# Kernel tuning notes

Hardware: AMD Instinct MI355X
Metric: run time of the kernel (lower is better)

## Reference

```python
import jax, jax.numpy as jnp
from jax import lax
import numpy as np

CHUNK = 64


def short_conv(x, w):
    # depthwise causal conv1d: x (B,L,D), w (D,K)
    L = x.shape[1]
    K = w.shape[1]
    xp = jnp.pad(x, ((0, 0), (K - 1, 0), (0, 0)))
    return sum(xp[:, j:j + L, :] * w[:, j] for j in range(K))


def o2b_weighted_delta_rule(k, q, v, b):
    # k,q,v,b: (B,L,H,D) float32, zero initial state
    B, L, H, D = k.shape
    C = CHUNK
    Nc = L // C

    def to_chunks(t):  # (B,L,H,D) -> (Nc,B,H,C,D)
        return t.transpose(0, 2, 1, 3).reshape(B, H, Nc, C, D).transpose(2, 0, 1, 3, 4)

    Kc, Qc, Vc, Bc = map(to_chunks, (k, q, v, b))
    eyeC = jnp.eye(C, dtype=jnp.float32)
    W0 = jnp.zeros((B, H, D, D), jnp.float32)
    Cf = float(C)

    def step(carry, xs):
        W_t, W_avg = carry
        i, Ki, Qi, Vi, Bi = xs
        KiT = jnp.swapaxes(Ki, -1, -2)
        T = jnp.tril(Bi @ KiT, k=-1)                      # (B,H,C,C) strictly lower
        inv = jnp.linalg.inv(eyeC + T)
        Ui = inv @ (Vi - Bi @ W_t)                        # (B,H,C,D)
        W_new = W_t + KiT @ Ui
        ts = (i * C).astype(jnp.float32)                  # init t == 0 for all batches
        idx = jnp.arange(1, C + 1, dtype=jnp.float32) + ts  # (C,)
        cs = jnp.cumsum(idx)
        weighted_idx = idx + idx.sum() - cs
        w_i = (weighted_idx / ((1 + ts + Cf) * (ts + Cf) / 2))[:, None]  # (C,1)
        coef1 = ts / (ts + Cf) * ((1 + ts) / (1 + ts + Cf))
        coef2 = Cf / (ts + Cf) * ((ts * 2 + 1 + Cf) / (1 + ts + Cf))
        W_avg_new = coef1 * W_avg + coef2 * W_t + KiT @ (Ui * w_i)
        tri0 = (1 + ts) * ts / 2
        a = (tri0 / (tri0 + cs))[:, None]                 # (C,1)
        c = 1.0 - a
        r = cs[:, None]                                   # (C,1)
        j_idx = (cs - idx)[None, :]                       # (1,C)
        T_mat = jnp.where(r >= j_idx, (r - j_idx) / (tri0 + r), 0.0)  # (C,C)
        O_i = (Qi @ W_avg) * a + (Qi @ W_t) * c + (T_mat * (Qi @ KiT)) @ Ui
        return (W_new, W_avg_new), O_i

    (_, _), O = lax.scan(step, (W0, W0), (jnp.arange(Nc), Kc, Qc, Vc, Bc))
    # O: (Nc,B,H,C,D) -> (B,L,H,D)
    return O.transpose(1, 2, 0, 3, 4).reshape(B, H, L, D).transpose(0, 2, 1, 3)


def setup_inputs() -> dict:
    key = jax.random.key(0)
    ks = jax.random.split(key, 9)
    B, L, Dm, H = 4, 2048, 1024, 16
    Dh, K = Dm // H, 4
    s = 0.02
    return {
        'x': jax.random.normal(ks[0], (B, L, Dm), jnp.float32),
        'Wk': s * jax.random.normal(ks[1], (Dm, Dm), jnp.float32),
        'bk': jnp.zeros((Dm,), jnp.float32),
        'Wq': s * jax.random.normal(ks[2], (Dm, Dm), jnp.float32),
        'bq': jnp.zeros((Dm,), jnp.float32),
        'Wv': s * jax.random.normal(ks[3], (Dm, Dm), jnp.float32),
        'bv': jnp.zeros((Dm,), jnp.float32),
        'Wbeta': s * jax.random.normal(ks[4], (H, Dm), jnp.float32),
        'bbeta': jnp.zeros((H,), jnp.float32),
        'conv_k': 0.1 * jax.random.normal(ks[5], (Dm, K), jnp.float32),
        'conv_q': 0.1 * jax.random.normal(ks[6], (Dm, K), jnp.float32),
        'conv_v': 0.1 * jax.random.normal(ks[7], (Dm, K), jnp.float32),
        'rms_w': jnp.ones((Dh,), jnp.float32),
        'Wout': s * jax.random.normal(ks[8], (Dm, Dm), jnp.float32),
        'bout': jnp.zeros((Dm,), jnp.float32),
    }


def reference(x, Wk, bk, Wq, bq, Wv, bv, Wbeta, bbeta, conv_k, conv_q, conv_v, rms_w, Wout, bout):
    B, L, Dm = x.shape
    H = Wbeta.shape[0]
    Dh = Dm // H
    k = short_conv(x @ Wk.T + bk, conv_k)
    q = short_conv(x @ Wq.T + bq, conv_q)
    v = short_conv(x @ Wv.T + bv, conv_v)
    beta = jax.nn.sigmoid(x @ Wbeta.T + bbeta)            # (B,L,H)
    k = k.reshape(B, L, H, Dh)
    q = q.reshape(B, L, H, Dh)
    v = jax.nn.silu(v.reshape(B, L, H, Dh))
    knorm = jnp.linalg.norm(k, axis=-1, keepdims=True)
    qnorm = jnp.linalg.norm(q, axis=-1, keepdims=True)
    k = k / (knorm + 1e-6)
    q = q / (qnorm + 1e-6)
    eta = beta  # eta coefficient = 1.0, ogd_mode='deltanet'
    b = eta[..., None] * k
    v = eta[..., None] * v
    o = o2b_weighted_delta_rule(k, q, v, b)               # (B,L,H,Dh)
    o = o * jax.lax.rsqrt(jnp.mean(o * o, axis=-1, keepdims=True) + 1e-6) * rms_w
    o = o.reshape(B, L, Dm)
    return o @ Wout.T + bout
```

## Files before the change

### kernel.cpp

```cpp
#include <hip/hip_runtime.h>

typedef __attribute__((ext_vector_type(8))) short bf16x8;
typedef __attribute__((ext_vector_type(4))) float f32x4;

#define MFMA(a, b, c) __builtin_amdgcn_mfma_f32_16x16x32_bf16((a), (b), (c), 0, 0, 0)

__device__ inline unsigned short f2bf_rne(float f) {
  unsigned int u = __float_as_uint(f);
  u += 0x7FFFu + ((u >> 16) & 1u);
  return (unsigned short)(u >> 16);
}

__global__ __launch_bounds__(256) void cast_bf16_kernel(const float* __restrict__ in,
                                                        unsigned short* __restrict__ out,
                                                        int n4) {
  const int i = blockIdx.x * 256 + threadIdx.x;
  if (i >= n4) return;
  const float4 v = ((const float4*)in)[i];
  ushort4 o;
  o.x = f2bf_rne(v.x); o.y = f2bf_rne(v.y); o.z = f2bf_rne(v.z); o.w = f2bf_rne(v.w);
  ((ushort4*)out)[i] = o;
}

__global__ __launch_bounds__(256) void gemm_bf16_nt(
    const unsigned short* __restrict__ A, const unsigned short* __restrict__ Bw,
    const float* __restrict__ bias, float* __restrict__ C, int M, int N, int K) {
  __shared__ unsigned short Asl[128 * 32];
  __shared__ unsigned short Bsl[128 * 32];
  const int tid = threadIdx.x;
  const int lane = tid & 63, w = tid >> 6;
  const int bm = blockIdx.x * 128, bn = blockIdx.y * 128;
  const int wr = (w >> 1) * 64, wc = (w & 1) * 64;

  const int li0 = tid, li1 = tid + 256;
  const int ar0 = li0 >> 2, ak0 = (li0 & 3) * 8;
  const int ar1 = li1 >> 2, ak1 = (li1 & 3) * 8;
  const unsigned short* gA0 = A + (size_t)(bm + ar0) * K + ak0;
  const unsigned short* gA1 = A + (size_t)(bm + ar1) * K + ak1;
  const unsigned short* gB0 = Bw + (size_t)(bn + ar0) * K + ak0;
  const unsigned short* gB1 = Bw + (size_t)(bn + ar1) * K + ak1;
  unsigned short* lA0 = &Asl[(size_t)(w * 64) * 8];
  unsigned short* lA1 = &Asl[(size_t)(w * 64 + 256) * 8];
  unsigned short* lB0 = &Bsl[(size_t)(w * 64) * 8];
  unsigned short* lB1 = &Bsl[(size_t)(w * 64 + 256) * 8];

  f32x4 acc[4][4];
#pragma unroll
  for (int i = 0; i < 4; ++i)
#pragma unroll
    for (int j = 0; j < 4; ++j) acc[i][j] = (f32x4){0.f, 0.f, 0.f, 0.f};

  const int fr = lane & 15, kg = lane >> 4;

  for (int k0 = 0; k0 < K; k0 += 32) {
    __syncthreads();
    __builtin_amdgcn_global_load_lds((const __attribute__((address_space(1))) unsigned int*)(gA0 + k0),
                                     (__attribute__((address_space(3))) unsigned int*)lA0, 16, 0, 0);
    __builtin_amdgcn_global_load_lds((const __attribute__((address_space(1))) unsigned int*)(gA1 + k0),
                                     (__attribute__((address_space(3))) unsigned int*)lA1, 16, 0, 0);
    __builtin_amdgcn_global_load_lds((const __attribute__((address_space(1))) unsigned int*)(gB0 + k0),
                                     (__attribute__((address_space(3))) unsigned int*)lB0, 16, 0, 0);
    __builtin_amdgcn_global_load_lds((const __attribute__((address_space(1))) unsigned int*)(gB1 + k0),
                                     (__attribute__((address_space(3))) unsigned int*)lB1, 16, 0, 0);
    __syncthreads();

    bf16x8 af[4], bfr[4];
#pragma unroll
    for (int i = 0; i < 4; ++i) {
      af[i] = *(const bf16x8*)&Asl[(size_t)(wr + i * 16 + fr) * 32 + kg * 8];
      bfr[i] = *(const bf16x8*)&Bsl[(size_t)(wc + i * 16 + fr) * 32 + kg * 8];
    }
#pragma unroll
    for (int i = 0; i < 4; ++i)
#pragma unroll
      for (int j = 0; j < 4; ++j)
        acc[i][j] = MFMA(af[i], bfr[j], acc[i][j]);
  }

  const int og = lane >> 4;
#pragma unroll
  for (int j = 0; j < 4; ++j) {
    const int col = bn + wc + j * 16 + fr;
    const float bs = bias[col];
#pragma unroll
    for (int i = 0; i < 4; ++i) {
#pragma unroll
      for (int r = 0; r < 4; ++r) {
        const int row = bm + wr + i * 16 + og * 4 + r;
        C[(size_t)row * N + col] = acc[i][j][r] + bs;
      }
    }
  }
}

__global__ __launch_bounds__(256) void beta_kernel(const float* __restrict__ x,
                                                   const float* __restrict__ Wb,
                                                   const float* __restrict__ bb,
                                                   float* __restrict__ beta) {
  const int m = blockIdx.x;
  const int tid = threadIdx.x;
  const int h = tid >> 4;
  const int l = tid & 15;
  const float4* x4 = (const float4*)(x + (size_t)m * 1024);
  const float4* w4 = (const float4*)(Wb + (size_t)h * 1024);
  float acc = 0.f;
#pragma unroll 4
  for (int jj = 0; jj < 16; ++jj) {
    float4 xv = x4[l + 16 * jj];
    float4 wv = w4[l + 16 * jj];
    acc += xv.x * wv.x + xv.y * wv.y + xv.z * wv.z + xv.w * wv.w;
  }
  acc += __shfl_xor(acc, 1);
  acc += __shfl_xor(acc, 2);
  acc += __shfl_xor(acc, 4);
  acc += __shfl_xor(acc, 8);
  if (l == 0) {
    const float s = acc + bb[h];
    beta[(size_t)m * 16 + h] = 1.f / (1.f + expf(-s));
  }
}

__global__ __launch_bounds__(256) void prep_kernel(
    const float* __restrict__ kpre, const float* __restrict__ qpre,
    const float* __restrict__ vpre, const float* __restrict__ betab,
    const float* __restrict__ convk, const float* __restrict__ convq,
    const float* __restrict__ convv,
    unsigned short* __restrict__ kn16, unsigned short* __restrict__ qn16,
    float* __restrict__ vz) {
  const int m = blockIdx.x;
  const int l = m & 2047;
  const int lane = threadIdx.x & 63;
  const int wvi = threadIdx.x >> 6;
#pragma unroll
  for (int s = 0; s < 4; ++s) {
    const int h = 4 * s + wvi;
    const int c = h * 64 + lane;
    const float4 wk4 = *(const float4*)(convk + (size_t)c * 4);
    const float4 wq4 = *(const float4*)(convq + (size_t)c * 4);
    const float4 wv4 = *(const float4*)(convv + (size_t)c * 4);
    const float wk[4] = {wk4.x, wk4.y, wk4.z, wk4.w};
    const float wq[4] = {wq4.x, wq4.y, wq4.z, wq4.w};
    const float wvv[4] = {wv4.x, wv4.y, wv4.z, wv4.w};
    float kc = 0.f, qc = 0.f, vc = 0.f;
#pragma unroll
    for (int j = 0; j < 4; ++j) {
      const int lj = l - 3 + j;
      if (lj >= 0) {
        const size_t base = ((size_t)(m - l + lj)) * 1024 + c;
        kc += wk[j] * kpre[base];
        qc += wq[j] * qpre[base];
        vc += wvv[j] * vpre[base];
      }
    }
    float ssk = kc * kc, ssq = qc * qc;
    ssk += __shfl_xor(ssk, 1); ssq += __shfl_xor(ssq, 1);
    ssk += __shfl_xor(ssk, 2); ssq += __shfl_xor(ssq, 2);
    ssk += __shfl_xor(ssk, 4); ssq += __shfl_xor(ssq, 4);
    ssk += __shfl_xor(ssk, 8); ssq += __shfl_xor(ssq, 8);
    ssk += __shfl_xor(ssk, 16); ssq += __shfl_xor(ssq, 16);
    ssk += __shfl_xor(ssk, 32); ssq += __shfl_xor(ssq, 32);
    const float eta = betab[(size_t)m * 16 + h];
    const size_t o = (size_t)m * 1024 + c;
    kn16[o] = f2bf_rne(kc / (sqrtf(ssk) + 1e-6f));
    qn16[o] = f2bf_rne(qc / (sqrtf(ssq) + 1e-6f));
    vz[o] = eta * vc / (1.f + expf(-vc));
  }
}

#define LDB 72
#define LDV 68

__global__ __launch_bounds__(512, 1) void scan_kernel(
    const unsigned short* __restrict__ kn16, const unsigned short* __restrict__ qn16,
    const float* __restrict__ vz, const float* __restrict__ betab,
    float* __restrict__ O) {
  __shared__ unsigned short Kb[64 * LDB], Qb[64 * LDB], Ktb[64 * LDB];
  __shared__ unsigned short Wtb[64 * LDB], Wavgtb[64 * LDB];
  __shared__ unsigned short Pb[64 * LDB], Ptb[64 * LDB], P1b[64 * LDB];
  __shared__ unsigned short Ztb[64 * LDB], Utwb[64 * LDB], Sbf[64 * LDB];
  __shared__ float Vs[64 * LDV];
  __shared__ float etas[64];

  const int tid = threadIdx.x;
  const int bh = blockIdx.x;
  const int b = bh >> 4, h = bh & 15;
  const int wv = tid >> 6, lane = tid & 63;
  const int fr = lane & 15, og = lane >> 4;
  const int i0 = (wv >> 2) * 2, i1 = i0 + 1, j = wv & 3;
  const int gcol = j * 16 + fr;
  const int row0 = i0 * 16 + og * 4;
  const int row1 = i1 * 16 + og * 4;

  for (int t = tid; t < 64 * LDB; t += 512) { Wtb[t] = 0; Wavgtb[t] = 0; }

  const size_t base = ((size_t)b * 2048) * 1024 + (size_t)h * 64;
  const unsigned short* kp = kn16 + base;
  const unsigned short* qp = qn16 + base;
  const float* vp = vz + base;
  const float* etap = betab + (size_t)b * 2048 * 16 + h;
  float* Op = O + (size_t)bh * 2048 * 64;

  f32x4 Wt[2], Wav[2];
  Wt[0] = Wt[1] = Wav[0] = Wav[1] = (f32x4){0.f, 0.f, 0.f, 0.f};

  const int sr = tid >> 3, sc8 = (tid & 7) * 8;
  __syncthreads();

#pragma unroll 1
  for (int ic = 0; ic < 32; ++ic) {
    const float ts = (float)(ic * 64);

    {
      const size_t g = (size_t)(ic * 64 + sr) * 1024 + sc8;
      *(ushort4*)&Kb[sr * LDB + sc8] = *(const ushort4*)(kp + g);
      *(ushort4*)&Kb[sr * LDB + sc8 + 4] = *(const ushort4*)(kp + g + 4);
      *(ushort4*)&Qb[sr * LDB + sc8] = *(const ushort4*)(qp + g);
      *(ushort4*)&Qb[sr * LDB + sc8 + 4] = *(const ushort4*)(qp + g + 4);
      *(float4*)&Vs[sr * LDV + sc8] = *(const float4*)(vp + g);
      *(float4*)&Vs[sr * LDV + sc8 + 4] = *(const float4*)(vp + g + 4);
      unsigned short tv[8];
#pragma unroll
      for (int i = 0; i < 8; ++i)
        tv[i] = kp[(size_t)(ic * 64 + sc8 + i) * 1024 + sr];
      ushort4 t0v = {tv[0], tv[1], tv[2], tv[3]}, t1v = {tv[4], tv[5], tv[6], tv[7]};
      *(ushort4*)&Ktb[sr * LDB + sc8] = t0v;
      *(ushort4*)&Ktb[sr * LDB + sc8 + 4] = t1v;
      if (tid < 64) etas[tid] = etap[(size_t)(ic * 64 + tid) * 16];
    }
    __syncthreads();

    f32x4 Zacc[2], RHSs[2];
    {
      bf16x8 aK0[2], aK1[2], bK[2], bW[2];
#pragma unroll
      for (int t = 0; t < 2; ++t) {
        aK0[t] = *(const bf16x8*)&Kb[(i0 * 16 + fr) * LDB + t * 32 + og * 8];
        aK1[t] = *(const bf16x8*)&Kb[(i1 * 16 + fr) * LDB + t * 32 + og * 8];
        bK[t] = *(const bf16x8*)&Kb[(j * 16 + fr) * LDB + t * 32 + og * 8];
        bW[t] = *(const bf16x8*)&Wtb[(j * 16 + fr) * LDB + t * 32 + og * 8];
      }
      f32x4 accT0 = {0, 0, 0, 0}, accT1 = {0, 0, 0, 0};
      f32x4 accR0 = {0, 0, 0, 0}, accR1 = {0, 0, 0, 0};
#pragma unroll
      for (int t = 0; t < 2; ++t) {
        accT0 = MFMA(aK0[t], bK[t], accT0);
        accT1 = MFMA(aK1[t], bK[t], accT1);
        accR0 = MFMA(aK0[t], bW[t], accR0);
        accR1 = MFMA(aK1[t], bW[t], accR1);
      }
#pragma unroll
      for (int s = 0; s < 2; ++s) {
        const int rb = s ? row1 : row0;
        const f32x4 aT = s ? accT1 : accT0;
        const f32x4 aR = s ? accR1 : accR0;
        unsigned short us[4];
        float zv[4];
#pragma unroll
        for (int r = 0; r < 4; ++r) {
          const int grow = rb + r;
          const float eta = etas[grow];
          const float tvv = (gcol < grow) ? -eta * aT[r] : 0.f;
          us[r] = f2bf_rne(tvv);
          zv[r] = Vs[grow * LDV + gcol] - eta * aR[r];
          Pb[grow * LDB + gcol] = us[r];
          P1b[grow * LDB + gcol] = us[r];
        }
        ushort4 pp = {us[0], us[1], us[2], us[3]};
        *(ushort4*)&Ptb[gcol * LDB + rb] = pp;
        ushort4 zp = {f2bf_rne(zv[0]), f2bf_rne(zv[1]), f2bf_rne(zv[2]), f2bf_rne(zv[3])};
        *(ushort4*)&Ztb[gcol * LDB + rb] = zp;
        Zacc[s] = (f32x4){zv[0], zv[1], zv[2], zv[3]};
        RHSs[s] = Zacc[s];
      }
    }
    __syncthreads();

    for (int k = 0; k < 6; ++k) {
      bf16x8 aP0[2], aP1[2], bZ[2];
#pragma unroll
      for (int t = 0; t < 2; ++t) {
        aP0[t] = *(const bf16x8*)&Pb[(i0 * 16 + fr) * LDB + t * 32 + og * 8];
        aP1[t] = *(const bf16x8*)&Pb[(i1 * 16 + fr) * LDB + t * 32 + og * 8];
        bZ[t] = *(const bf16x8*)&Ztb[(j * 16 + fr) * LDB + t * 32 + og * 8];
      }
      f32x4 sq0 = {0, 0, 0, 0}, sq1 = {0, 0, 0, 0};
      if (k < 5) {
#pragma unroll
        for (int t = 0; t < 2; ++t) {
          bf16x8 bPt = *(const bf16x8*)&Ptb[(j * 16 + fr) * LDB + t * 32 + og * 8];
          sq0 = MFMA(aP0[t], bPt, sq0);
          sq1 = MFMA(aP1[t], bPt, sq1);
        }
      }
#pragma unroll
      for (int t = 0; t < 2; ++t) {
        Zacc[0] = MFMA(aP0[t], bZ[t], Zacc[0]);
        Zacc[1] = MFMA(aP1[t], bZ[t], Zacc[1]);
      }
      __syncthreads();
#pragma unroll
      for (int s = 0; s < 2; ++s) {
        const int rb = s ? row1 : row0;
        const f32x4 zz = Zacc[s];
        ushort4 zp = {f2bf_rne(zz[0]), f2bf_rne(zz[1]), f2bf_rne(zz[2]), f2bf_rne(zz[3])};
        *(ushort4*)&Ztb[gcol * LDB + rb] = zp;
        if (k < 5) {
          const f32x4 sv = s ? sq1 : sq0;
          unsigned short u0 = f2bf_rne(sv[0]), u1 = f2bf_rne(sv[1]);
          unsigned short u2 = f2bf_rne(sv[2]), u3 = f2bf_rne(sv[3]);
          Pb[(rb + 0) * LDB + gcol] = u0;
          Pb[(rb + 1) * LDB + gcol] = u1;
          Pb[(rb + 2) * LDB + gcol] = u2;
          Pb[(rb + 3) * LDB + gcol] = u3;
          ushort4 pp = {u0, u1, u2, u3};
          *(ushort4*)&Ptb[gcol * LDB + rb] = pp;
        }
      }
      __syncthreads();
    }

    {
      bf16x8 a0[2], a1[2];
#pragma unroll
      for (int t = 0; t < 2; ++t) {
        a0[t] = *(const bf16x8*)&P1b[(i0 * 16 + fr) * LDB + t * 32 + og * 8];
        a1[t] = *(const bf16x8*)&P1b[(i1 * 16 + fr) * LDB + t * 32 + og * 8];
      }
      f32x4 R0 = RHSs[0] - Zacc[0];
      f32x4 R1 = RHSs[1] - Zacc[1];
#pragma unroll
      for (int t = 0; t < 2; ++t) {
        bf16x8 bU = *(const bf16x8*)&Ztb[(j * 16 + fr) * LDB + t * 32 + og * 8];
        R0 = MFMA(a0[t], bU, R0);
        R1 = MFMA(a1[t], bU, R1);
      }
      ushort4 r0p = {f2bf_rne(R0[0]), f2bf_rne(R0[1]), f2bf_rne(R0[2]), f2bf_rne(R0[3])};
      ushort4 r1p = {f2bf_rne(R1[0]), f2bf_rne(R1[1]), f2bf_rne(R1[2]), f2bf_rne(R1[3])};
      *(ushort4*)&Sbf[gcol * LDB + row0] = r0p;
      *(ushort4*)&Sbf[gcol * LDB + row1] = r1p;
      __syncthreads();
      f32x4 dU0 = R0, dU1 = R1;
#pragma unroll
      for (int t = 0; t < 2; ++t) {
        bf16x8 bR = *(const bf16x8*)&Sbf[(j * 16 + fr) * LDB + t * 32 + og * 8];
        dU0 = MFMA(a0[t], bR, dU0);
        dU1 = MFMA(a1[t], bR, dU1);
      }
      Zacc[0] += dU0;
      Zacc[1] += dU1;
      const float invden = 1.f / (0.5f * (ts + 65.f) * (ts + 64.f));
#pragma unroll
      for (int s = 0; s < 2; ++s) {
        const int rb = s ? row1 : row0;
        const f32x4 uu = Zacc[s];
        ushort4 up = {f2bf_rne(uu[0]), f2bf_rne(uu[1]), f2bf_rne(uu[2]), f2bf_rne(uu[3])};
        *(ushort4*)&Ztb[gcol * LDB + rb] = up;
        unsigned short uw[4];
#pragma unroll
        for (int r = 0; r < 4; ++r) {
          const float rr = (float)(rb + r);
          const float wr = (ts * (64.f - rr) + (rr + 1.f) + 2080.f -
                            0.5f * (rr + 1.f) * (rr + 2.f)) * invden;
          uw[r] = f2bf_rne(uu[r] * wr);
        }
        ushort4 uwp = {uw[0], uw[1], uw[2], uw[3]};
        *(ushort4*)&Utwb[gcol * LDB + rb] = uwp;
      }
      __syncthreads();
    }

    f32x4 Oacc[2];
    {
      bf16x8 aQ0[2], aQ1[2], bKj[2], bWt2[2], bWa2[2];
#pragma unroll
      for (int t = 0; t < 2; ++t) {
        aQ0[t] = *(const bf16x8*)&Qb[(i0 * 16 + fr) * LDB + t * 32 + og * 8];
        aQ1[t] = *(const bf16x8*)&Qb[(i1 * 16 + fr) * LDB + t * 32 + og * 8];
        bKj[t] = *(const bf16x8*)&Kb[(j * 16 + fr) * LDB + t * 32 + og * 8];
        bWt2[t] = *(const bf16x8*)&Wtb[(j * 16 + fr) * LDB + t * 32 + og * 8];
        bWa2[t] = *(const bf16x8*)&Wavgtb[(j * 16 + fr) * LDB + t * 32 + og * 8];
      }
      f32x4 aS0 = {0, 0, 0, 0}, aS1 = {0, 0, 0, 0};
      f32x4 aA0 = {0, 0, 0, 0}, aA1 = {0, 0, 0, 0};
      f32x4 aC0 = {0, 0, 0, 0}, aC1 = {0, 0, 0, 0};
#pragma unroll
      for (int t = 0; t < 2; ++t) {
        aS0 = MFMA(aQ0[t], bKj[t], aS0);
        aS1 = MFMA(aQ1[t], bKj[t], aS1);
        aA0 = MFMA(aQ0[t], bWa2[t], aA0);
        aA1 = MFMA(aQ1[t], bWa2[t], aA1);
        aC0 = MFMA(aQ0[t], bWt2[t], aC0);
        aC1 = MFMA(aQ1[t], bWt2[t], aC1);
      }
      const float tri0 = 0.5f * ts * (ts + 1.f);
      const float jidx = gcol * ts + 0.5f * gcol * (gcol + 1.f);
#pragma unroll
      for (int s = 0; s < 2; ++s) {
        const int rb = s ? row1 : row0;
        const f32x4 sS = s ? aS1 : aS0;
        const f32x4 sA = s ? aA1 : aA0;
        const f32x4 sC = s ? aC1 : aC0;
        f32x4 oo;
#pragma unroll
        for (int r = 0; r < 4; ++r) {
          const float grow = (float)(rb + r);
          const float csr = (grow + 1.f) * ts + 0.5f * (grow + 1.f) * (grow + 2.f);
          const float rinv = 1.f / (tri0 + csr);
          const float av = tri0 * rinv;
          oo[r] = av * sA[r] + (1.f - av) * sC[r];
          const float svv = (csr >= jidx) ? (csr - jidx) * rinv * sS[r] : 0.f;
          Sbf[(rb + r) * LDB + gcol] = f2bf_rne(svv);
        }
        Oacc[s] = oo;
      }
    }
    __syncthreads();

    {
      bf16x8 aS0[2], aS1[2], bU2[2];
#pragma unroll
      for (int t = 0; t < 2; ++t) {
        aS0[t] = *(const bf16x8*)&Sbf[(i0 * 16 + fr) * LDB + t * 32 + og * 8];
        aS1[t] = *(const bf16x8*)&Sbf[(i1 * 16 + fr) * LDB + t * 32 + og * 8];
        bU2[t] = *(const bf16x8*)&Ztb[(j * 16 + fr) * LDB + t * 32 + og * 8];
      }
#pragma unroll
      for (int t = 0; t < 2; ++t) {
        Oacc[0] = MFMA(aS0[t], bU2[t], Oacc[0]);
        Oacc[1] = MFMA(aS1[t], bU2[t], Oacc[1]);
      }
#pragma unroll
      for (int s = 0; s < 2; ++s) {
        const int rb = s ? row1 : row0;
#pragma unroll
        for (int r = 0; r < 4; ++r)
          Op[(size_t)(ic * 64 + rb + r) * 64 + gcol] = Oacc[s][r];
      }
    }

    {
      bf16x8 aU0[2], aU1[2], aW0[2], aW1[2], bKt2[2];
#pragma unroll
      for (int t = 0; t < 2; ++t) {
        aU0[t] = *(const bf16x8*)&Ztb[(i0 * 16 + fr) * LDB + t * 32 + og * 8];
        aU1[t] = *(const bf16x8*)&Ztb[(i1 * 16 + fr) * LDB + t * 32 + og * 8];
        aW0[t] = *(const bf16x8*)&Utwb[(i0 * 16 + fr) * LDB + t * 32 + og * 8];
        aW1[t] = *(const bf16x8*)&Utwb[(i1 * 16 + fr) * LDB + t * 32 + og * 8];
        bKt2[t] = *(const bf16x8*)&Ktb[(j * 16 + fr) * LDB + t * 32 + og * 8];
      }
      const float den = (ts + 64.f) * (ts + 65.f);
      const float cc1 = ts * (ts + 1.f) / den;
      const float cc2 = 64.f * (2.f * ts + 65.f) / den;
      f32x4 wn0 = cc1 * Wav[0] + cc2 * Wt[0];
      f32x4 wn1 = cc1 * Wav[1] + cc2 * Wt[1];
#pragma unroll
      for (int t = 0; t < 2; ++t) {
        wn0 = MFMA(aW0[t], bKt2[t], wn0);
        wn1 = MFMA(aW1[t], bKt2[t], wn1);
        Wt[0] = MFMA(aU0[t], bKt2[t], Wt[0]);
        Wt[1] = MFMA(aU1[t], bKt2[t], Wt[1]);
      }
      Wav[0] = wn0;
      Wav[1] = wn1;
#pragma unroll
      for (int s = 0; s < 2; ++s) {
        const int rb = s ? row1 : row0;
        const f32x4 wtv = Wt[s];
        const f32x4 wav2 = Wav[s];
#pragma unroll
        for (int r = 0; r < 4; ++r) {
          Wtb[(rb + r) * LDB + gcol] = f2bf_rne(wtv[r]);
          Wavgtb[(rb + r) * LDB + gcol] = f2bf_rne(wav2[r]);
        }
      }
    }
    __syncthreads();
  }
}

__global__ __launch_bounds__(256) void rms_kernel(const float* __restrict__ O,
                                                  const float* __restrict__ rmsw,
                                                  unsigned short* __restrict__ out16) {
  const int m = blockIdx.x;
  const int b = m >> 11, l = m & 2047;
  const int wv = threadIdx.x >> 6, lane = threadIdx.x & 63;
  const float rw = rmsw[lane];
#pragma unroll
  for (int hh = 0; hh < 4; ++hh) {
    const int h = wv * 4 + hh;
    const float v = O[(((size_t)(b * 16 + h)) * 2048 + l) * 64 + lane];
    float ss = v * v;
    ss += __shfl_xor(ss, 1); ss += __shfl_xor(ss, 2); ss += __shfl_xor(ss, 4);
    ss += __shfl_xor(ss, 8); ss += __shfl_xor(ss, 16); ss += __shfl_xor(ss, 32);
    const float sc = rsqrtf(ss * (1.f / 64.f) + 1e-6f);
    out16[(size_t)m * 1024 + h * 64 + lane] = f2bf_rne(v * sc * rw);
  }
}

extern "C" void kernel_launch(void* const* d_in, const int* in_sizes, int n_in,
                              void* d_out, int out_size, void* d_ws, size_t ws_size,
                              hipStream_t stream) {
  (void)in_sizes; (void)n_in; (void)out_size; (void)ws_size;
  const float* x     = (const float*)d_in[0];
  const float* Wk    = (const float*)d_in[1];
  const float* bk    = (const float*)d_in[2];
  const float* Wq    = (const float*)d_in[3];
  const float* bq    = (const float*)d_in[4];
  const float* Wv    = (const float*)d_in[5];
  const float* bv    = (const float*)d_in[6];
  const float* Wbeta = (const float*)d_in[7];
  const float* bbeta = (const float*)d_in[8];
  const float* convk = (const float*)d_in[9];
  const float* convq = (const float*)d_in[10];
  const float* convv = (const float*)d_in[11];
  const float* rmsw  = (const float*)d_in[12];
  const float* Wout  = (const float*)d_in[13];
  const float* bout  = (const float*)d_in[14];
  float* out = (float*)d_out;
  float* ws = (float*)d_ws;

  const size_t SZ = (size_t)8192 * 1024;
  float* kpre = ws;
  float* qpre = ws + SZ;
  float* vpre = ws + 2 * SZ;
  float* betab = ws + 3 * SZ;
  unsigned short* x16 = (unsigned short*)(ws + 3 * SZ + 131072);
  unsigned short* wk16 = x16 + SZ;
  unsigned short* wq16 = wk16 + 1048576;
  unsigned short* wv16 = wq16 + 1048576;
  unsigned short* wo16 = wv16 + 1048576;
  unsigned short* kn16 = wo16 + 1048576;
  unsigned short* qn16 = kn16 + SZ;
  float* vzb = out;
  float* Obuf = kpre;
  unsigned short* normed16 = (unsigned short*)qpre;

  dim3 blk(256);
  hipLaunchKernelGGL(cast_bf16_kernel, dim3(8192), blk, 0, stream, x, x16, (int)(SZ / 4));
  hipLaunchKernelGGL(cast_bf16_kernel, dim3(1024), blk, 0, stream, Wk, wk16, 262144);
  hipLaunchKernelGGL(cast_bf16_kernel, dim3(1024), blk, 0, stream, Wq, wq16, 262144);
  hipLaunchKernelGGL(cast_bf16_kernel, dim3(1024), blk, 0, stream, Wv, wv16, 262144);
  hipLaunchKernelGGL(cast_bf16_kernel, dim3(1024), blk, 0, stream, Wout, wo16, 262144);

  dim3 g(64, 8);
  hipLaunchKernelGGL(gemm_bf16_nt, g, blk, 0, stream, x16, wk16, bk, kpre, 8192, 1024, 1024);
  hipLaunchKernelGGL(gemm_bf16_nt, g, blk, 0, stream, x16, wq16, bq, qpre, 8192, 1024, 1024);
  hipLaunchKernelGGL(gemm_bf16_nt, g, blk, 0, stream, x16, wv16, bv, vpre, 8192, 1024, 1024);
  hipLaunchKernelGGL(beta_kernel, dim3(8192), blk, 0, stream, x, Wbeta, bbeta, betab);
  hipLaunchKernelGGL(prep_kernel, dim3(8192), blk, 0, stream, kpre, qpre, vpre, betab,
                     convk, convq, convv, kn16, qn16, vzb);
  hipLaunchKernelGGL(scan_kernel, dim3(64), dim3(512), 0, stream, kn16, qn16, vzb,
                     betab, Obuf);
  hipLaunchKernelGGL(rms_kernel, dim3(8192), blk, 0, stream, Obuf, rmsw, normed16);
  hipLaunchKernelGGL(gemm_bf16_nt, g, blk, 0, stream, normed16, wo16, bout, out,
                     8192, 1024, 1024);
}
```

Measured before the change: 626.5 us.

## Fuse QKV projections into one GEMM and double-buffer scan LDS to drop barriers

The three K/Q/V projection GEMMs are merged into a single N=3072 GEMM writing an interleaved qkv buffer, with a small kernel concatenating the biases, and prep_kernel reads from that layout. This relies on wk16/wq16/wv16 being contiguous so they act as one 3072x1024 weight matrix. In the scan kernel, the Neumann-series inverse loop now double-buffers the P/Pt/Z shared tiles, removing one __syncthreads per iteration. Scratch buffers are reused to fit the extra LDS buffers, and one barrier after the U/Utw writes is also removed, which risks a race if later readers depended on it.

```diff
diff --git a/kernel.cpp b/kernel.cpp
--- a/kernel.cpp
+++ b/kernel.cpp
@@ -20,6 +20,16 @@
   ushort4 o;
   o.x = f2bf_rne(v.x); o.y = f2bf_rne(v.y); o.z = f2bf_rne(v.z); o.w = f2bf_rne(v.w);
   ((ushort4*)out)[i] = o;
+}
+
+__global__ __launch_bounds__(256) void concat_bias_kernel(const float* __restrict__ bk,
+                                                          const float* __restrict__ bq,
+                                                          const float* __restrict__ bv,
+                                                          float* __restrict__ b3) {
+  const int i = blockIdx.x * 256 + threadIdx.x;
+  if (i < 1024) b3[i] = bk[i];
+  else if (i < 2048) b3[i] = bq[i - 1024];
+  else if (i < 3072) b3[i] = bv[i - 2048];
 }
 
 __global__ __launch_bounds__(256) void gemm_bf16_nt(
@@ -121,8 +131,7 @@
 }
 
 __global__ __launch_bounds__(256) void prep_kernel(
-    const float* __restrict__ kpre, const float* __restrict__ qpre,
-    const float* __restrict__ vpre, const float* __restrict__ betab,
+    const float* __restrict__ qkv, const float* __restrict__ betab,
     const float* __restrict__ convk, const float* __restrict__ convq,
     const float* __restrict__ convv,
     unsigned short* __restrict__ kn16, unsigned short* __restrict__ qn16,
@@ -146,10 +155,10 @@
     for (int j = 0; j < 4; ++j) {
       const int lj = l - 3 + j;
       if (lj >= 0) {
-        const size_t base = ((size_t)(m - l + lj)) * 1024 + c;
-        kc += wk[j] * kpre[base];
-        qc += wq[j] * qpre[base];
-        vc += wvv[j] * vpre[base];
+        const size_t rb = (size_t)(m - l + lj) * 3072 + c;
+        kc += wk[j] * qkv[rb];
+        qc += wq[j] * qkv[rb + 1024];
+        vc += wvv[j] * qkv[rb + 2048];
       }
     }
     float ssk = kc * kc, ssq = qc * qc;
@@ -176,8 +185,8 @@
     float* __restrict__ O) {
   __shared__ unsigned short Kb[64 * LDB], Qb[64 * LDB], Ktb[64 * LDB];
   __shared__ unsigned short Wtb[64 * LDB], Wavgtb[64 * LDB];
-  __shared__ unsigned short Pb[64 * LDB], Ptb[64 * LDB], P1b[64 * LDB];
-  __shared__ unsigned short Ztb[64 * LDB], Utwb[64 * LDB], Sbf[64 * LDB];
+  __shared__ unsigned short Pb[2][64 * LDB], Ptb[2][64 * LDB], Ztb[2][64 * LDB];
+  __shared__ unsigned short P1b[64 * LDB], Utwb[64 * LDB];
   __shared__ float Vs[64 * LDV];
   __shared__ float etas[64];
 
@@ -262,32 +271,34 @@
           const float tvv = (gcol < grow) ? -eta * aT[r] : 0.f;
           us[r] = f2bf_rne(tvv);
           zv[r] = Vs[grow * LDV + gcol] - eta * aR[r];
-          Pb[grow * LDB + gcol] = us[r];
+          Pb[0][grow * LDB + gcol] = us[r];
           P1b[grow * LDB + gcol] = us[r];
         }
         ushort4 pp = {us[0], us[1], us[2], us[3]};
-        *(ushort4*)&Ptb[gcol * LDB + rb] = pp;
+        *(ushort4*)&Ptb[0][gcol * LDB + rb] = pp;
         ushort4 zp = {f2bf_rne(zv[0]), f2bf_rne(zv[1]), f2bf_rne(zv[2]), f2bf_rne(zv[3])};
-        *(ushort4*)&Ztb[gcol * LDB + rb] = zp;
+        *(ushort4*)&Ztb[0][gcol * LDB + rb] = zp;
         Zacc[s] = (f32x4){zv[0], zv[1], zv[2], zv[3]};
         RHSs[s] = Zacc[s];
       }
     }
     __syncthreads();
 
+#pragma unroll
     for (int k = 0; k < 6; ++k) {
+      const int cur = k & 1, nxt = cur ^ 1;
       bf16x8 aP0[2], aP1[2], bZ[2];
 #pragma unroll
       for (int t = 0; t < 2; ++t) {
-        aP0[t] = *(const bf16x8*)&Pb[(i0 * 16 + fr) * LDB + t * 32 + og * 8];
-        aP1[t] = *(const bf16x8*)&Pb[(i1 * 16 + fr) * LDB + t * 32 + og * 8];
-        bZ[t] = *(const bf16x8*)&Ztb[(j * 16 + fr) * LDB + t * 32 + og * 8];
+        aP0[t] = *(const bf16x8*)&Pb[cur][(i0 * 16 + fr) * LDB + t * 32 + og * 8];
+        aP1[t] = *(const bf16x8*)&Pb[cur][(i1 * 16 + fr) * LDB + t * 32 + og * 8];
+        bZ[t] = *(const bf16x8*)&Ztb[cur][(j * 16 + fr) * LDB + t * 32 + og * 8];
       }
       f32x4 sq0 = {0, 0, 0, 0}, sq1 = {0, 0, 0, 0};
       if (k < 5) {
 #pragma unroll
         for (int t = 0; t < 2; ++t) {
-          bf16x8 bPt = *(const bf16x8*)&Ptb[(j * 16 + fr) * LDB + t * 32 + og * 8];
+          bf16x8 bPt = *(const bf16x8*)&Ptb[cur][(j * 16 + fr) * LDB + t * 32 + og * 8];
           sq0 = MFMA(aP0[t], bPt, sq0);
           sq1 = MFMA(aP1[t], bPt, sq1);
         }
@@ -297,30 +308,29 @@
         Zacc[0] = MFMA(aP0[t], bZ[t], Zacc[0]);
         Zacc[1] = MFMA(aP1[t], bZ[t], Zacc[1]);
       }
-      __syncthreads();
 #pragma unroll
       for (int s = 0; s < 2; ++s) {
         const int rb = s ? row1 : row0;
         const f32x4 zz = Zacc[s];
         ushort4 zp = {f2bf_rne(zz[0]), f2bf_rne(zz[1]), f2bf_rne(zz[2]), f2bf_rne(zz[3])};
-        *(ushort4*)&Ztb[gcol * LDB + rb] = zp;
+        *(ushort4*)&Ztb[nxt][gcol * LDB + rb] = zp;
         if (k < 5) {
           const f32x4 sv = s ? sq1 : sq0;
           unsigned short u0 = f2bf_rne(sv[0]), u1 = f2bf_rne(sv[1]);
           unsigned short u2 = f2bf_rne(sv[2]), u3 = f2bf_rne(sv[3]);
-          Pb[(rb + 0) * LDB + gcol] = u0;
-          Pb[(rb + 1) * LDB + gcol] = u1;
-          Pb[(rb + 2) * LDB + gcol] = u2;
-          Pb[(rb + 3) * LDB + gcol] = u3;
+          Pb[nxt][(rb + 0) * LDB + gcol] = u0;
+          Pb[nxt][(rb + 1) * LDB + gcol] = u1;
+          Pb[nxt][(rb + 2) * LDB + gcol] = u2;
+          Pb[nxt][(rb + 3) * LDB + gcol] = u3;
           ushort4 pp = {u0, u1, u2, u3};
-          *(ushort4*)&Ptb[gcol * LDB + rb] = pp;
+          *(ushort4*)&Ptb[nxt][gcol * LDB + rb] = pp;
         }
       }
       __syncthreads();
     }
 
-    {
-      bf16x8 a0[2], a1[2];
+    bf16x8 a0[2], a1[2];
+    {
 #pragma unroll
       for (int t = 0; t < 2; ++t) {
         a0[t] = *(const bf16x8*)&P1b[(i0 * 16 + fr) * LDB + t * 32 + og * 8];
@@ -330,19 +340,24 @@
       f32x4 R1 = RHSs[1] - Zacc[1];
 #pragma unroll
       for (int t = 0; t < 2; ++t) {
-        bf16x8 bU = *(const bf16x8*)&Ztb[(j * 16 + fr) * LDB + t * 32 + og * 8];
+        bf16x8 bU = *(const bf16x8*)&Ztb[0][(j * 16 + fr) * LDB + t * 32 + og * 8];
         R0 = MFMA(a0[t], bU, R0);
         R1 = MFMA(a1[t], bU, R1);
       }
       ushort4 r0p = {f2bf_rne(R0[0]), f2bf_rne(R0[1]), f2bf_rne(R0[2]), f2bf_rne(R0[3])};
       ushort4 r1p = {f2bf_rne(R1[0]), f2bf_rne(R1[1]), f2bf_rne(R1[2]), f2bf_rne(R1[3])};
-      *(ushort4*)&Sbf[gcol * LDB + row0] = r0p;
-      *(ushort4*)&Sbf[gcol * LDB + row1] = r1p;
-      __syncthreads();
-      f32x4 dU0 = R0, dU1 = R1;
-#pragma unroll
-      for (int t = 0; t < 2; ++t) {
-        bf16x8 bR = *(const bf16x8*)&Sbf[(j * 16 + fr) * LDB + t * 32 + og * 8];
+      *(ushort4*)&Pb[1][gcol * LDB + row0] = r0p;
+      *(ushort4*)&Pb[1][gcol * LDB + row1] = r1p;
+      RHSs[0] = R0;
+      RHSs[1] = R1;
+    }
+    __syncthreads();
+
+    {
+      f32x4 dU0 = RHSs[0], dU1 = RHSs[1];
+#pragma unroll
+      for (int t = 0; t < 2; ++t) {
+        bf16x8 bR = *(const bf16x8*)&Pb[1][(j * 16 + fr) * LDB + t * 32 + og * 8];
         dU0 = MFMA(a0[t], bR, dU0);
         dU1 = MFMA(a1[t], bR, dU1);
       }
@@ -354,7 +369,7 @@
         const int rb = s ? row1 : row0;
         const f32x4 uu = Zacc[s];
         ushort4 up = {f2bf_rne(uu[0]), f2bf_rne(uu[1]), f2bf_rne(uu[2]), f2bf_rne(uu[3])};
-        *(ushort4*)&Ztb[gcol * LDB + rb] = up;
+        *(ushort4*)&Ztb[0][gcol * LDB + rb] = up;
         unsigned short uw[4];
 #pragma unroll
         for (int r = 0; r < 4; ++r) {
@@ -366,9 +381,7 @@
         ushort4 uwp = {uw[0], uw[1], uw[2], uw[3]};
         *(ushort4*)&Utwb[gcol * LDB + rb] = uwp;
       }
-      __syncthreads();
-    }
-
+    }
     f32x4 Oacc[2];
     {
       bf16x8 aQ0[2], aQ1[2], bKj[2], bWt2[2], bWa2[2];
@@ -409,7 +422,7 @@
           const float av = tri0 * rinv;
           oo[r] = av * sA[r] + (1.f - av) * sC[r];
           const float svv = (csr >= jidx) ? (csr - jidx) * rinv * sS[r] : 0.f;
-          Sbf[(rb + r) * LDB + gcol] = f2bf_rne(svv);
+          Ptb[1][(rb + r) * LDB + gcol] = f2bf_rne(svv);
         }
         Oacc[s] = oo;
       }
@@ -420,9 +433,9 @@
       bf16x8 aS0[2], aS1[2], bU2[2];
 #pragma unroll
       for (int t = 0; t < 2; ++t) {
-        aS0[t] = *(const bf16x8*)&Sbf[(i0 * 16 + fr) * LDB + t * 32 + og * 8];
-        aS1[t] = *(const bf16x8*)&Sbf[(i1 * 16 + fr) * LDB + t * 32 + og * 8];
-        bU2[t] = *(const bf16x8*)&Ztb[(j * 16 + fr) * LDB + t * 32 + og * 8];
+        aS0[t] = *(const bf16x8*)&Ptb[1][(i0 * 16 + fr) * LDB + t * 32 + og * 8];
+        aS1[t] = *(const bf16x8*)&Ptb[1][(i1 * 16 + fr) * LDB + t * 32 + og * 8];
+        bU2[t] = *(const bf16x8*)&Ztb[0][(j * 16 + fr) * LDB + t * 32 + og * 8];
       }
 #pragma unroll
       for (int t = 0; t < 2; ++t) {
@@ -442,8 +455,8 @@
       bf16x8 aU0[2], aU1[2], aW0[2], aW1[2], bKt2[2];
 #pragma unroll
       for (int t = 0; t < 2; ++t) {
-        aU0[t] = *(const bf16x8*)&Ztb[(i0 * 16 + fr) * LDB + t * 32 + og * 8];
-        aU1[t] = *(const bf16x8*)&Ztb[(i1 * 16 + fr) * LDB + t * 32 + og * 8];
+        aU0[t] = *(const bf16x8*)&Ztb[0][(i0 * 16 + fr) * LDB + t * 32 + og * 8];
+        aU1[t] = *(const bf16x8*)&Ztb[0][(i1 * 16 + fr) * LDB + t * 32 + og * 8];
         aW0[t] = *(const bf16x8*)&Utwb[(i0 * 16 + fr) * LDB + t * 32 + og * 8];
         aW1[t] = *(const bf16x8*)&Utwb[(i1 * 16 + fr) * LDB + t * 32 + og * 8];
         bKt2[t] = *(const bf16x8*)&Ktb[(j * 16 + fr) * LDB + t * 32 + og * 8];
@@ -520,9 +533,7 @@
   float* ws = (float*)d_ws;
 
   const size_t SZ = (size_t)8192 * 1024;
-  float* kpre = ws;
-  float* qpre = ws + SZ;
-  float* vpre = ws + 2 * SZ;
+  float* qkv = ws;
   float* betab = ws + 3 * SZ;
   unsigned short* x16 = (unsigned short*)(ws + 3 * SZ + 131072);
   unsigned short* wk16 = x16 + SZ;
@@ -531,9 +542,10 @@
   unsigned short* wo16 = wv16 + 1048576;
   unsigned short* kn16 = wo16 + 1048576;
   unsigned short* qn16 = kn16 + SZ;
+  float* b3 = (float*)(qn16 + SZ);
   float* vzb = out;
-  float* Obuf = kpre;
-  unsigned short* normed16 = (unsigned short*)qpre;
+  float* Obuf = qkv;
+  unsigned short* normed16 = (unsigned short*)(ws + SZ);
 
   dim3 blk(256);
   hipLaunchKernelGGL(cast_bf16_kernel, dim3(8192), blk, 0, stream, x, x16, (int)(SZ / 4));
@@ -541,17 +553,16 @@
   hipLaunchKernelGGL(cast_bf16_kernel, dim3(1024), blk, 0, stream, Wq, wq16, 262144);
   hipLaunchKernelGGL(cast_bf16_kernel, dim3(1024), blk, 0, stream, Wv, wv16, 262144);
   hipLaunchKernelGGL(cast_bf16_kernel, dim3(1024), blk, 0, stream, Wout, wo16, 262144);
-
-  dim3 g(64, 8);
-  hipLaunchKernelGGL(gemm_bf16_nt, g, blk, 0, stream, x16, wk16, bk, kpre, 8192, 1024, 1024);
-  hipLaunchKernelGGL(gemm_bf16_nt, g, blk, 0, stream, x16, wq16, bq, qpre, 8192, 1024, 1024);
-  hipLaunchKernelGGL(gemm_bf16_nt, g, blk, 0, stream, x16, wv16, bv, vpre, 8192, 1024, 1024);
+  hipLaunchKernelGGL(concat_bias_kernel, dim3(12), blk, 0, stream, bk, bq, bv, b3);
+
+  hipLaunchKernelGGL(gemm_bf16_nt, dim3(64, 24), blk, 0, stream, x16, wk16, b3,
+                     qkv, 8192, 3072, 1024);
   hipLaunchKernelGGL(beta_kernel, dim3(8192), blk, 0, stream, x, Wbeta, bbeta, betab);
-  hipLaunchKernelGGL(prep_kernel, dim3(8192), blk, 0, stream, kpre, qpre, vpre, betab,
+  hipLaunchKernelGGL(prep_kernel, dim3(8192), blk, 0, stream, qkv, betab,
                      convk, convq, convv, kn16, qn16, vzb);
   hipLaunchKernelGGL(scan_kernel, dim3(64), dim3(512), 0, stream, kn16, qn16, vzb,
                      betab, Obuf);
   hipLaunchKernelGGL(rms_kernel, dim3(8192), blk, 0, stream, Obuf, rmsw, normed16);
-  hipLaunchKernelGGL(gemm_bf16_nt, g, blk, 0, stream, normed16, wo16, bout, out,
+  hipLaunchKernelGGL(gemm_bf16_nt, dim3(64, 8), blk, 0, stream, normed16, wo16, bout, out,
                      8192, 1024, 1024);
 }
```

After: 586.1 us. -6.5%, faster.
